# Optimization experiments

Measured on AMD Instinct MI355X. Metric: run time of the kernel, lower is better.

The kernel has to match this reference:

```python
import jax, jax.numpy as jnp
import numpy as np

B, N, DIM = 2, 2048, 1024
HEADS, DIM_HEAD = 16, 64
INNER = HEADS * DIM_HEAD  # 1024
SCALE = DIM_HEAD ** -0.5


def setup_inputs() -> dict:
    key = jax.random.key(0)
    ks = jax.random.split(key, 6)
    s = lambda k, shape, fan: jax.random.normal(k, shape, jnp.float32) * (fan ** -0.5)
    return {
        "x": jax.random.normal(ks[0], (B, N, DIM), jnp.float32),
        "similarity": jax.random.normal(ks[1], (B, N), jnp.float32),
        "Wq": s(ks[2], (DIM, INNER), DIM),
        "Wkv": s(ks[3], (DIM, 2 * INNER), DIM),
        "Wo": s(ks[4], (INNER, DIM), INNER),
        "bo": jnp.zeros((DIM,), jnp.float32),
    }


def reference(x, similarity, Wq, Wkv, Wo, bo):
    b, n, _ = x.shape
    h, d = HEADS, DIM_HEAD
    # projections (context = x, self-attention)
    q = (x @ Wq).reshape(b, n, h, d).transpose(0, 2, 1, 3)        # b h n d
    kv = x @ Wkv                                                   # b n 2*inner
    k, v = jnp.split(kv, 2, axis=-1)
    k = k.reshape(b, n, h, d).transpose(0, 2, 1, 3)
    v = v.reshape(b, n, h, d).transpose(0, 2, 1, 3)
    dots = jnp.einsum('bhid,bhjd->bhij', q, k) * SCALE             # b h n n
    # similarity [b,n] -> broadcast as per-query row bias [b,1,n,1]
    dots = dots + similarity[:, None, :, None]
    attn = jax.nn.softmax(dots, axis=-1)
    out = jnp.einsum('bhij,bhjd->bhid', attn, v)                   # b h n d
    out = out.transpose(0, 2, 1, 3).reshape(b, n, h * d)           # b n inner
    return out @ Wo + bo
```

## Files before the change

### kernel.cpp

```cpp
#include <hip/hip_runtime.h>


typedef __attribute__((ext_vector_type(8))) short short8;
typedef __attribute__((ext_vector_type(4))) float float4_;
typedef __attribute__((ext_vector_type(16))) float floatx16;
typedef __attribute__((ext_vector_type(4))) unsigned short ushort4_;
typedef __attribute__((ext_vector_type(4))) unsigned int uint4_;

#define MFMA(a, b, c) __builtin_amdgcn_mfma_f32_16x16x32_bf16((a), (b), (c), 0, 0, 0)
#define MFMA32(a, b, c) __builtin_amdgcn_mfma_f32_32x32x16_bf16((a), (b), (c), 0, 0, 0)

static __device__ __forceinline__ unsigned short f2bf(float f) {
    union { float f; unsigned int u; } v; v.f = f;
    unsigned int r = v.u + 0x7FFFu + ((v.u >> 16) & 1u);
    return (unsigned short)(r >> 16);
}

static __device__ __forceinline__ void gld16(const void* g, void* l) {
    __builtin_amdgcn_global_load_lds(
        (__attribute__((address_space(1))) void*)(g),
        (__attribute__((address_space(3))) void*)(l), 16, 0, 0);
}

__global__ __launch_bounds__(256) void prep(
    const float* __restrict__ X, const float* __restrict__ Wq,
    const float* __restrict__ Wkv, const float* __restrict__ Wo,
    unsigned short* __restrict__ xb, unsigned short* __restrict__ Wt,
    unsigned short* __restrict__ Wot)
{
    const int bid = blockIdx.x, t = threadIdx.x;
    if (bid >= 1024) {
        const int b = bid - 1024;
        const float4_* src = (const float4_*)X;
        ushort4_* dst = (ushort4_*)xb;
        #pragma unroll
        for (int g = 0; g < 8; ++g) {
            const int idx = b * 2048 + g * 256 + t;
            float4_ v = src[idx];
            ushort4_ o;
            o[0] = f2bf(v[0]); o[1] = f2bf(v[1]);
            o[2] = f2bf(v[2]); o[3] = f2bf(v[3]);
            dst[idx] = o;
        }
        return;
    }
    __shared__ float tile[64][65];
    const float* src; unsigned short* dst; int N, kt, nt, drow0;
    if (bid < 256)      { src = Wq;  N = 1024; kt = bid & 15;       nt = bid >> 4;       dst = Wt;  drow0 = nt * 64; }
    else if (bid < 768) { src = Wkv; N = 2048; kt = (bid-256) & 15; nt = (bid-256) >> 4; dst = Wt;  drow0 = 1024 + nt * 64; }
    else                { src = Wo;  N = 1024; kt = (bid-768) & 15; nt = (bid-768) >> 4; dst = Wot; drow0 = nt * 64; }
    const int k0 = kt * 64, n0 = nt * 64;
    const int r0 = t >> 6, c = t & 63;
    #pragma unroll
    for (int i = 0; i < 16; ++i) {
        const int r = i * 4 + r0;
        tile[r][c] = src[(size_t)(k0 + r) * N + n0 + c];
    }
    __syncthreads();
    #pragma unroll
    for (int i = 0; i < 16; ++i) {
        const int rn = i * 4 + r0;
        dst[(size_t)(drow0 + rn) * 1024 + k0 + c] = f2bf(tile[c][rn]);
    }
}

__global__ __launch_bounds__(256) void qkv_gemm2(
    const unsigned short* __restrict__ xb, const unsigned short* __restrict__ Wt,
    unsigned short* __restrict__ q_ws, unsigned short* __restrict__ k_ws,
    unsigned short* __restrict__ vt_ws)
{
    __shared__ unsigned short As[128 * 64];
    __shared__ unsigned short Bs[128 * 64];
    const int t = threadIdx.x, wave = t >> 6, lane = t & 63;
    const int L = lane & 15, quad = lane >> 4;
    const int mb = blockIdx.x / 24, nb = blockIdx.x % 24;
    const int m0 = mb * 128, n0 = nb * 128;
    const int wr = wave >> 1, wc = wave & 1;

    float4_ z = {0.f, 0.f, 0.f, 0.f};
    float4_ acc[4][4];
    #pragma unroll
    for (int i = 0; i < 4; ++i)
        #pragma unroll
        for (int j = 0; j < 4; ++j) acc[i][j] = z;

    const unsigned short* gA[4]; const unsigned short* gB[4];
    unsigned short* lA[4]; unsigned short* lB[4];
    #pragma unroll
    for (int j = 0; j < 4; ++j) {
        const int cid = wave * 256 + j * 64 + lane;
        const int row = cid >> 3, pc = cid & 7;
        const int lch = pc ^ (row & 7);
        gA[j] = xb + (size_t)(m0 + row) * 1024 + lch * 8;
        gB[j] = Wt + (size_t)(n0 + row) * 1024 + lch * 8;
        lA[j] = As + wave * 2048 + j * 512;
        lB[j] = Bs + wave * 2048 + j * 512;
    }

    for (int kc = 0; kc < 1024; kc += 64) {
        #pragma unroll
        for (int j = 0; j < 4; ++j) {
            gld16(gA[j] + kc, lA[j]);
            gld16(gB[j] + kc, lB[j]);
        }
        __syncthreads();
        #pragma unroll
        for (int ks = 0; ks < 2; ++ks) {
            short8 af[4], bfr[4];
            #pragma unroll
            for (int mt = 0; mt < 4; ++mt) {
                const int rl = wr * 64 + mt * 16 + L;
                af[mt] = *(const short8*)(As + rl * 64 + (((ks * 4 + quad) ^ (L & 7)) << 3));
            }
            #pragma unroll
            for (int nt = 0; nt < 4; ++nt) {
                const int rl = wc * 64 + nt * 16 + L;
                bfr[nt] = *(const short8*)(Bs + rl * 64 + (((ks * 4 + quad) ^ (L & 7)) << 3));
            }
            #pragma unroll
            for (int mt = 0; mt < 4; ++mt)
                #pragma unroll
                for (int nt = 0; nt < 4; ++nt)
                    acc[mt][nt] = MFMA(af[mt], bfr[nt], acc[mt][nt]);
        }
        __syncthreads();
    }

    const int b = m0 >> 11;
    const int type = n0 >> 10;
    #pragma unroll
    for (int mt = 0; mt < 4; ++mt) {
        const int m = (m0 & 2047) + wr * 64 + mt * 16 + quad * 4;
        #pragma unroll
        for (int nt = 0; nt < 4; ++nt) {
            const int cl = (n0 & 1023) + wc * 64 + nt * 16 + L;
            const int h = cl >> 6, d = cl & 63;
            float4_ v = acc[mt][nt];
            if (type == 0) {
                unsigned short* p = q_ws + ((size_t)(b * 16 + h) * 2048 + m) * 64 + d;
                #pragma unroll
                for (int r = 0; r < 4; ++r) p[(size_t)r * 64] = f2bf(v[r] * 0.18033688011f);
            } else if (type == 1) {
                unsigned short* p = k_ws + ((size_t)(b * 16 + h) * 2048 + m) * 64 + d;
                #pragma unroll
                for (int r = 0; r < 4; ++r) p[(size_t)r * 64] = f2bf(v[r]);
            } else {
                ushort4_ pk;
                pk[0] = f2bf(v[0]); pk[1] = f2bf(v[1]);
                pk[2] = f2bf(v[2]); pk[3] = f2bf(v[3]);
                *(ushort4_*)(vt_ws + ((size_t)(b * 16 + h) * 64 + d) * 2048 + m) = pk;
            }
        }
    }
}

__global__ __launch_bounds__(256) void attn_fwd3(
    const unsigned short* __restrict__ q_ws,
    const unsigned short* __restrict__ k_ws,
    const unsigned short* __restrict__ vt_ws,
    unsigned short* __restrict__ o2)
{
    __shared__ unsigned short k_lds[2][64 * 64];
    __shared__ unsigned short v_lds[2][64 * 64];
    __shared__ float ls[4][32];
    const int t = threadIdx.x, wave = t >> 6, lane = t & 63;
    const int l32 = lane & 31, hi = lane >> 5;
    const int bh = blockIdx.x >> 4, qb = blockIdx.x & 15;

    const unsigned short* Kp = k_ws + (size_t)bh * 2048 * 64;
    const unsigned short* Vt = vt_ws + (size_t)bh * 64 * 2048;

    const unsigned short* Qp = q_ws + ((size_t)bh * 2048 + qb * 128 + wave * 32 + l32) * 64;
    short8 qf[4];
    #pragma unroll
    for (int s = 0; s < 4; ++s) qf[s] = *(const short8*)(Qp + hi * 8 + s * 16);

    const int c0 = wave * 64 + lane;
    const int kr0 = c0 >> 3, kl0 = (c0 & 7) ^ (kr0 & 7);
    const int kr1 = kr0 + 32;
    const unsigned short* ks0 = Kp + (size_t)kr0 * 64 + kl0 * 8;
    const unsigned short* ks1 = Kp + (size_t)kr1 * 64 + kl0 * 8;
    const unsigned short* vs0 = Vt + (size_t)kr0 * 2048 + kl0 * 8;
    const unsigned short* vs1 = Vt + (size_t)kr1 * 2048 + kl0 * 8;
    const int dst0 = wave * 512, dst1 = 2048 + wave * 512;

    floatx16 o0, o1;
    #pragma unroll
    for (int r = 0; r < 16; ++r) { o0[r] = 0.f; o1[r] = 0.f; }
    float lsum = 0.f;

    gld16(ks0, k_lds[0] + dst0); gld16(ks1, k_lds[0] + dst1);
    gld16(vs0, v_lds[0] + dst0); gld16(vs1, v_lds[0] + dst1);
    __syncthreads();

    const int sw = l32 & 7;
    for (int j0 = 0; j0 < 2048; j0 += 64) {
        const int p = (j0 >> 6) & 1;
        if (j0 + 64 < 2048) {
            const int np = p ^ 1;
            gld16(ks0 + (j0 + 64) * 64, k_lds[np] + dst0);
            gld16(ks1 + (j0 + 64) * 64, k_lds[np] + dst1);
            gld16(vs0 + (j0 + 64), v_lds[np] + dst0);
            gld16(vs1 + (j0 + 64), v_lds[np] + dst1);
        }
        const unsigned short* kb = k_lds[p];
        const unsigned short* vb = v_lds[p];

        floatx16 s0, s1;
        #pragma unroll
        for (int r = 0; r < 16; ++r) { s0[r] = 0.f; s1[r] = 0.f; }
        #pragma unroll
        for (int s = 0; s < 4; ++s) {
            const int lch = 2 * s + hi;
            short8 k0 = *(const short8*)(kb + l32 * 64 + ((lch ^ sw) << 3));
            short8 k1 = *(const short8*)(kb + (32 + l32) * 64 + ((lch ^ sw) << 3));
            s0 = MFMA32(k0, qf[s], s0);
            s1 = MFMA32(k1, qf[s], s1);
        }

        unsigned int pk0[8], pk1[8];
        #pragma unroll
        for (int d = 0; d < 8; ++d) {
            union { float f; unsigned int u; } a0, b0, a1, b1;
            a0.f = __builtin_amdgcn_exp2f(s0[2 * d]);
            b0.f = __builtin_amdgcn_exp2f(s0[2 * d + 1]);
            a1.f = __builtin_amdgcn_exp2f(s1[2 * d]);
            b1.f = __builtin_amdgcn_exp2f(s1[2 * d + 1]);
            lsum += (a0.f + b0.f) + (a1.f + b1.f);
            pk0[d] = (a0.u >> 16) | (b0.u & 0xFFFF0000u);
            pk1[d] = (a1.u >> 16) | (b1.u & 0xFFFF0000u);
        }

        #pragma unroll
        for (int w = 0; w < 4; ++w) {
            uint4_ pw;
            if (w == 0)      { pw[0] = pk0[0]; pw[1] = pk0[1]; pw[2] = pk0[2]; pw[3] = pk0[3]; }
            else if (w == 1) { pw[0] = pk0[4]; pw[1] = pk0[5]; pw[2] = pk0[6]; pw[3] = pk0[7]; }
            else if (w == 2) { pw[0] = pk1[0]; pw[1] = pk1[1]; pw[2] = pk1[2]; pw[3] = pk1[3]; }
            else             { pw[0] = pk1[4]; pw[1] = pk1[5]; pw[2] = pk1[6]; pw[3] = pk1[7]; }
            short8 pa = *(short8*)&pw;

            const unsigned short* vr0 = vb + l32 * 64;
            const unsigned short* vr1 = vb + (32 + l32) * 64;
            const int ca = (((2 * w) ^ sw) << 3) + 4 * hi;
            const int cb = (((2 * w + 1) ^ sw) << 3) + 4 * hi;
            ushort4_ va0 = *(const ushort4_*)(vr0 + ca);
            ushort4_ vb0 = *(const ushort4_*)(vr0 + cb);
            ushort4_ va1 = *(const ushort4_*)(vr1 + ca);
            ushort4_ vb1 = *(const ushort4_*)(vr1 + cb);
            short8 vf0, vf1;
            #pragma unroll
            for (int i = 0; i < 4; ++i) {
                vf0[i] = (short)va0[i]; vf0[4 + i] = (short)vb0[i];
                vf1[i] = (short)va1[i]; vf1[4 + i] = (short)vb1[i];
            }
            o0 = MFMA32(pa, vf0, o0);
            o1 = MFMA32(pa, vf1, o1);
        }
        __syncthreads();
    }

    float ltot = lsum + __shfl_xor(lsum, 32);
    ls[wave][l32] = ltot;
    float inv[16];
    #pragma unroll
    for (int r = 0; r < 16; ++r)
        inv[r] = 1.0f / ls[wave][(r & 3) + 8 * (r >> 2) + 4 * hi];

    const int b = bh >> 4, h = bh & 15;
    unsigned short* ob = o2 + ((size_t)b * 2048 + qb * 128 + wave * 32) * 1024 + h * 64;
    #pragma unroll
    for (int r = 0; r < 16; ++r) {
        const int row = (r & 3) + 8 * (r >> 2) + 4 * hi;
        ob[(size_t)row * 1024 + l32]      = f2bf(o0[r] * inv[r]);
        ob[(size_t)row * 1024 + 32 + l32] = f2bf(o1[r] * inv[r]);
    }
}

__global__ __launch_bounds__(256) void out_gemm2(
    const unsigned short* __restrict__ o2, const unsigned short* __restrict__ Wot,
    const float* __restrict__ bo, float* __restrict__ Out)
{
    __shared__ unsigned short As[128 * 64];
    __shared__ unsigned short Bs[64 * 64];
    const int t = threadIdx.x, wave = t >> 6, lane = t & 63;
    const int L = lane & 15, quad = lane >> 4;
    const int mb = blockIdx.x >> 4, nb = blockIdx.x & 15;
    const int m0 = mb * 128, n0 = nb * 64;
    const int wr = wave >> 1, wc = wave & 1;

    float4_ z = {0.f, 0.f, 0.f, 0.f};
    float4_ acc[4][2];
    #pragma unroll
    for (int i = 0; i < 4; ++i)
        #pragma unroll
        for (int j = 0; j < 2; ++j) acc[i][j] = z;

    const unsigned short* gA[4]; unsigned short* lA[4];
    #pragma unroll
    for (int j = 0; j < 4; ++j) {
        const int cid = wave * 256 + j * 64 + lane;
        const int row = cid >> 3, pc = cid & 7;
        gA[j] = o2 + (size_t)(m0 + row) * 1024 + (pc ^ (row & 7)) * 8;
        lA[j] = As + wave * 2048 + j * 512;
    }
    const unsigned short* gB[2]; unsigned short* lB[2];
    #pragma unroll
    for (int j = 0; j < 2; ++j) {
        const int cid = wave * 128 + j * 64 + lane;
        const int row = cid >> 3, pc = cid & 7;
        gB[j] = Wot + (size_t)(n0 + row) * 1024 + (pc ^ (row & 7)) * 8;
        lB[j] = Bs + wave * 1024 + j * 512;
    }

    for (int kc = 0; kc < 1024; kc += 64) {
        #pragma unroll
        for (int j = 0; j < 4; ++j) gld16(gA[j] + kc, lA[j]);
        #pragma unroll
        for (int j = 0; j < 2; ++j) gld16(gB[j] + kc, lB[j]);
        __syncthreads();
        #pragma unroll
        for (int ks = 0; ks < 2; ++ks) {
            short8 af[4], bfr[2];
            #pragma unroll
            for (int mt = 0; mt < 4; ++mt) {
                const int rl = wr * 64 + mt * 16 + L;
                af[mt] = *(const short8*)(As + rl * 64 + (((ks * 4 + quad) ^ (L & 7)) << 3));
            }
            #pragma unroll
            for (int nt = 0; nt < 2; ++nt) {
                const int rl = wc * 32 + nt * 16 + L;
                bfr[nt] = *(const short8*)(Bs + rl * 64 + (((ks * 4 + quad) ^ (L & 7)) << 3));
            }
            #pragma unroll
            for (int mt = 0; mt < 4; ++mt)
                #pragma unroll
                for (int nt = 0; nt < 2; ++nt)
                    acc[mt][nt] = MFMA(af[mt], bfr[nt], acc[mt][nt]);
        }
        __syncthreads();
    }

    #pragma unroll
    for (int mt = 0; mt < 4; ++mt) {
        const int m = m0 + wr * 64 + mt * 16 + quad * 4;
        #pragma unroll
        for (int nt = 0; nt < 2; ++nt) {
            const int c = n0 + wc * 32 + nt * 16 + L;
            const float bias = bo[c];
            #pragma unroll
            for (int r = 0; r < 4; ++r)
                Out[(size_t)(m + r) * 1024 + c] = acc[mt][nt][r] + bias;
        }
    }
}

extern "C" void kernel_launch(void* const* d_in, const int* in_sizes, int n_in,
                              void* d_out, int out_size, void* d_ws, size_t ws_size,
                              hipStream_t stream) {
    const float* x   = (const float*)d_in[0];
    const float* Wq  = (const float*)d_in[2];
    const float* Wkv = (const float*)d_in[3];
    const float* Wo  = (const float*)d_in[4];
    const float* bo  = (const float*)d_in[5];
    float* out = (float*)d_out;

    char* ws = (char*)d_ws;
    const size_t MB = 1024 * 1024;
    unsigned short* xb   = (unsigned short*)(ws);
    unsigned short* o2   = xb;
    unsigned short* Wt   = (unsigned short*)(ws + 8 * MB);
    unsigned short* Wot  = (unsigned short*)(ws + 14 * MB);
    unsigned short* q_ws = (unsigned short*)(ws + 16 * MB);
    unsigned short* k_ws = (unsigned short*)(ws + 24 * MB);
    unsigned short* vt_ws= (unsigned short*)(ws + 32 * MB);

    prep<<<dim3(1536), dim3(256), 0, stream>>>(x, Wq, Wkv, Wo, xb, Wt, Wot);
    qkv_gemm2<<<dim3(768), dim3(256), 0, stream>>>(xb, Wt, q_ws, k_ws, vt_ws);
    attn_fwd3<<<dim3(512), dim3(256), 0, stream>>>(q_ws, k_ws, vt_ws, o2);
    out_gemm2<<<dim3(512), dim3(256), 0, stream>>>(o2, Wot, bo, out);
}
```

Baseline: 198.1 us.

## Split attention KV range across two blocks with flag-based combine

Splits each attention query tile's KV sequence into two halves, each processed by a separate block. The first block to finish writes unnormalized partial output and row sums to workspace and signals a counter; the second block spin-waits, adds the partial results, and normalizes. Blocks are also remapped so each XCD handles a contiguous set of heads, and K rows are permuted so V can be read with single 16-byte LDS loads instead of split 8-byte loads. Occupancy is hinted at 4 blocks per SIMD. The change doubles the grid for better CU fill at the cost of a memset, a spin-wait, and bf16 rounding of the partial output.

```diff
diff --git a/kernel.cpp b/kernel.cpp
--- a/kernel.cpp
+++ b/kernel.cpp
@@ -14,6 +14,10 @@
     union { float f; unsigned int u; } v; v.f = f;
     unsigned int r = v.u + 0x7FFFu + ((v.u >> 16) & 1u);
     return (unsigned short)(r >> 16);
+}
+static __device__ __forceinline__ float bf2f(unsigned short h) {
+    union { unsigned int u; float f; } v; v.u = ((unsigned int)h) << 16;
+    return v.f;
 }
 
 static __device__ __forceinline__ void gld16(const void* g, void* l) {
@@ -154,18 +158,44 @@
     }
 }
 
-__global__ __launch_bounds__(256) void attn_fwd3(
+__global__ __launch_bounds__(256, 4) void attn_fwd4(
     const unsigned short* __restrict__ q_ws,
     const unsigned short* __restrict__ k_ws,
     const unsigned short* __restrict__ vt_ws,
-    unsigned short* __restrict__ o2)
+    unsigned short* __restrict__ o2,
+    float* __restrict__ pL,
+    unsigned int* __restrict__ flags,
+    const int splits)
 {
     __shared__ unsigned short k_lds[2][64 * 64];
     __shared__ unsigned short v_lds[2][64 * 64];
     __shared__ float ls[4][32];
+    __shared__ int role_s;
     const int t = threadIdx.x, wave = t >> 6, lane = t & 63;
     const int l32 = lane & 31, hi = lane >> 5;
-    const int bh = blockIdx.x >> 4, qb = blockIdx.x & 15;
+
+    int bh, qb, s;
+    if (splits == 2) {
+        const int xcd = blockIdx.x & 7, loc = blockIdx.x >> 3;
+        bh = xcd * 4 + (loc >> 5);
+        const int rem = loc & 31;
+        qb = rem >> 1; s = rem & 1;
+    } else {
+        const int xcd = blockIdx.x & 7, loc = blockIdx.x >> 3;
+        bh = xcd * 4 + (loc >> 4);
+        qb = loc & 15; s = 0;
+    }
+    const int slot = bh * 16 + qb;
+
+    int role = 2;
+    if (splits == 2) {
+        if (t == 0) role_s = (int)atomicAdd(&flags[slot], 1u);
+        __syncthreads();
+        role = role_s;
+    }
+
+    const int j_lo = s * 1024;
+    const int iters = (splits == 2) ? 16 : 32;
 
     const unsigned short* Kp = k_ws + (size_t)bh * 2048 * 64;
     const unsigned short* Vt = vt_ws + (size_t)bh * 64 * 2048;
@@ -173,15 +203,15 @@
     const unsigned short* Qp = q_ws + ((size_t)bh * 2048 + qb * 128 + wave * 32 + l32) * 64;
     short8 qf[4];
     #pragma unroll
-    for (int s = 0; s < 4; ++s) qf[s] = *(const short8*)(Qp + hi * 8 + s * 16);
+    for (int k = 0; k < 4; ++k) qf[k] = *(const short8*)(Qp + hi * 8 + k * 16);
 
     const int c0 = wave * 64 + lane;
     const int kr0 = c0 >> 3, kl0 = (c0 & 7) ^ (kr0 & 7);
-    const int kr1 = kr0 + 32;
-    const unsigned short* ks0 = Kp + (size_t)kr0 * 64 + kl0 * 8;
-    const unsigned short* ks1 = Kp + (size_t)kr1 * 64 + kl0 * 8;
-    const unsigned short* vs0 = Vt + (size_t)kr0 * 2048 + kl0 * 8;
-    const unsigned short* vs1 = Vt + (size_t)kr1 * 2048 + kl0 * 8;
+    const int pr0 = (kr0 & ~12) | ((kr0 & 4) << 1) | ((kr0 & 8) >> 1);
+    const unsigned short* ks0 = Kp + (size_t)(j_lo + pr0) * 64 + kl0 * 8;
+    const unsigned short* ks1 = ks0 + 32 * 64;
+    const unsigned short* vs0 = Vt + (size_t)kr0 * 2048 + j_lo + kl0 * 8;
+    const unsigned short* vs1 = Vt + (size_t)(kr0 + 32) * 2048 + j_lo + kl0 * 8;
     const int dst0 = wave * 512, dst1 = 2048 + wave * 512;
 
     floatx16 o0, o1;
@@ -194,14 +224,15 @@
     __syncthreads();
 
     const int sw = l32 & 7;
-    for (int j0 = 0; j0 < 2048; j0 += 64) {
-        const int p = (j0 >> 6) & 1;
-        if (j0 + 64 < 2048) {
+    for (int it = 0; it < iters; ++it) {
+        const int p = it & 1;
+        if (it + 1 < iters) {
             const int np = p ^ 1;
-            gld16(ks0 + (j0 + 64) * 64, k_lds[np] + dst0);
-            gld16(ks1 + (j0 + 64) * 64, k_lds[np] + dst1);
-            gld16(vs0 + (j0 + 64), v_lds[np] + dst0);
-            gld16(vs1 + (j0 + 64), v_lds[np] + dst1);
+            const int joff = (it + 1) * 64;
+            gld16(ks0 + (size_t)joff * 64, k_lds[np] + dst0);
+            gld16(ks1 + (size_t)joff * 64, k_lds[np] + dst1);
+            gld16(vs0 + joff, v_lds[np] + dst0);
+            gld16(vs1 + joff, v_lds[np] + dst1);
         }
         const unsigned short* kb = k_lds[p];
         const unsigned short* vb = v_lds[p];
@@ -210,12 +241,12 @@
         #pragma unroll
         for (int r = 0; r < 16; ++r) { s0[r] = 0.f; s1[r] = 0.f; }
         #pragma unroll
-        for (int s = 0; s < 4; ++s) {
-            const int lch = 2 * s + hi;
+        for (int k = 0; k < 4; ++k) {
+            const int lch = 2 * k + hi;
             short8 k0 = *(const short8*)(kb + l32 * 64 + ((lch ^ sw) << 3));
             short8 k1 = *(const short8*)(kb + (32 + l32) * 64 + ((lch ^ sw) << 3));
-            s0 = MFMA32(k0, qf[s], s0);
-            s1 = MFMA32(k1, qf[s], s1);
+            s0 = MFMA32(k0, qf[k], s0);
+            s1 = MFMA32(k1, qf[k], s1);
         }
 
         unsigned int pk0[8], pk1[8];
@@ -239,21 +270,9 @@
             else if (w == 2) { pw[0] = pk1[0]; pw[1] = pk1[1]; pw[2] = pk1[2]; pw[3] = pk1[3]; }
             else             { pw[0] = pk1[4]; pw[1] = pk1[5]; pw[2] = pk1[6]; pw[3] = pk1[7]; }
             short8 pa = *(short8*)&pw;
-
-            const unsigned short* vr0 = vb + l32 * 64;
-            const unsigned short* vr1 = vb + (32 + l32) * 64;
-            const int ca = (((2 * w) ^ sw) << 3) + 4 * hi;
-            const int cb = (((2 * w + 1) ^ sw) << 3) + 4 * hi;
-            ushort4_ va0 = *(const ushort4_*)(vr0 + ca);
-            ushort4_ vb0 = *(const ushort4_*)(vr0 + cb);
-            ushort4_ va1 = *(const ushort4_*)(vr1 + ca);
-            ushort4_ vb1 = *(const ushort4_*)(vr1 + cb);
-            short8 vf0, vf1;
-            #pragma unroll
-            for (int i = 0; i < 4; ++i) {
-                vf0[i] = (short)va0[i]; vf0[4 + i] = (short)vb0[i];
-                vf1[i] = (short)va1[i]; vf1[4 + i] = (short)vb1[i];
-            }
+            const int c = 2 * w + hi;
+            short8 vf0 = *(const short8*)(vb + l32 * 64 + ((c ^ sw) << 3));
+            short8 vf1 = *(const short8*)(vb + (32 + l32) * 64 + ((c ^ sw) << 3));
             o0 = MFMA32(pa, vf0, o0);
             o1 = MFMA32(pa, vf1, o1);
         }
@@ -261,14 +280,44 @@
     }
 
     float ltot = lsum + __shfl_xor(lsum, 32);
-    ls[wave][l32] = ltot;
+    const int b = bh >> 4, h = bh & 15;
+    unsigned short* ob = o2 + ((size_t)b * 2048 + qb * 128 + wave * 32) * 1024 + h * 64;
+
+    if (role == 0) {
+        if (hi == 0) pL[slot * 128 + wave * 32 + l32] = ltot;
+        #pragma unroll
+        for (int r = 0; r < 16; ++r) {
+            const int row = (r & 3) + 8 * (r >> 2) + 4 * hi;
+            ob[(size_t)row * 1024 + l32]      = f2bf(o0[r]);
+            ob[(size_t)row * 1024 + 32 + l32] = f2bf(o1[r]);
+        }
+        __threadfence();
+        __syncthreads();
+        if (t == 0) atomicAdd(&flags[slot], 1u);
+        return;
+    }
+
+    if (role == 1) {
+        if (t == 0) {
+            while (atomicAdd(&flags[slot], 0u) < 3u) __builtin_amdgcn_s_sleep(8);
+        }
+        __syncthreads();
+        __threadfence();
+        ls[wave][l32] = ltot + pL[slot * 128 + wave * 32 + l32];
+        #pragma unroll
+        for (int r = 0; r < 16; ++r) {
+            const int row = (r & 3) + 8 * (r >> 2) + 4 * hi;
+            o0[r] += bf2f(ob[(size_t)row * 1024 + l32]);
+            o1[r] += bf2f(ob[(size_t)row * 1024 + 32 + l32]);
+        }
+    } else {
+        ls[wave][l32] = ltot;
+    }
+
     float inv[16];
     #pragma unroll
     for (int r = 0; r < 16; ++r)
         inv[r] = 1.0f / ls[wave][(r & 3) + 8 * (r >> 2) + 4 * hi];
-
-    const int b = bh >> 4, h = bh & 15;
-    unsigned short* ob = o2 + ((size_t)b * 2048 + qb * 128 + wave * 32) * 1024 + h * 64;
     #pragma unroll
     for (int r = 0; r < 16; ++r) {
         const int row = (r & 3) + 8 * (r >> 2) + 4 * hi;
@@ -374,9 +423,17 @@
     unsigned short* q_ws = (unsigned short*)(ws + 16 * MB);
     unsigned short* k_ws = (unsigned short*)(ws + 24 * MB);
     unsigned short* vt_ws= (unsigned short*)(ws + 32 * MB);
+    float*        pL     = (float*)(ws + 40 * MB);
+    unsigned int* flags  = (unsigned int*)(ws + 40 * MB + 256 * 1024);
+
+    const int splits = (ws_size >= 40 * MB + 272 * 1024) ? 2 : 1;
+
+    if (splits == 2)
+        hipMemsetAsync(flags, 0, 2048, stream);
 
     prep<<<dim3(1536), dim3(256), 0, stream>>>(x, Wq, Wkv, Wo, xb, Wt, Wot);
     qkv_gemm2<<<dim3(768), dim3(256), 0, stream>>>(xb, Wt, q_ws, k_ws, vt_ws);
-    attn_fwd3<<<dim3(512), dim3(256), 0, stream>>>(q_ws, k_ws, vt_ws, o2);
+    attn_fwd4<<<dim3(512 * splits), dim3(256), 0, stream>>>(q_ws, k_ws, vt_ws, o2,
+                                                            pL, flags, splits);
     out_gemm2<<<dim3(512), dim3(256), 0, stream>>>(o2, Wot, bo, out);
 }
```

New measurement: 309.5 us. 56.3% more time.
